# Kernel tuning notes

Hardware: AMD Instinct MI355X
Metric: run time of the kernel (lower is better)

Reference implementation:

```python
import jax, jax.numpy as jnp
import numpy as np

N = 32768       # total nodes = NUM_GRAPHS * T
F_IN = 32       # num_features
HC = 64         # hidden_channels
HEADS = 4
E = 524288      # edges before self-loops
NUM_GRAPHS = 64 # == batch.max()+1 by construction
T = 512         # time steps per graph (N // NUM_GRAPHS)
OUT = 24        # output_size
NEG_SLOPE = 0.2 # PyG GATConv default


def gat_layer(x, src, dst, W, a_src, a_dst, b, n_nodes):
    """PyG GATConv (concat=True) with edge softmax over incoming edges."""
    H, C = a_src.shape
    h = (x @ W).reshape(n_nodes, H, C)                    # [N,H,C]
    alpha_src = jnp.sum(h * a_src, axis=-1)               # [N,H]
    alpha_dst = jnp.sum(h * a_dst, axis=-1)               # [N,H]
    e = jax.nn.leaky_relu(alpha_src[src] + alpha_dst[dst], NEG_SLOPE)  # [E,H]
    m = jax.ops.segment_max(e, dst, num_segments=n_nodes)
    e = jnp.exp(e - m[dst])
    s = jax.ops.segment_sum(e, dst, num_segments=n_nodes)
    alpha = e / (s[dst] + 1e-16)                          # [E,H]
    msg = h[src] * alpha[..., None]                       # [E,H,C]
    out = jax.ops.segment_sum(msg, dst, num_segments=n_nodes)  # [N,H,C]
    return out.reshape(n_nodes, H * C) + b


def gru_layer(x, Wih, Whh, bih, bhh):
    """torch nn.GRU single layer, batch_first input x: [B,T,Hin] -> ([B,T,H], h_T)."""
    Bsz = x.shape[0]
    H = Whh.shape[1]

    def step(h, xt):
        gi = xt @ Wih.T + bih
        gh = h @ Whh.T + bhh
        ir, iz, inn = jnp.split(gi, 3, axis=-1)
        hr, hz, hn = jnp.split(gh, 3, axis=-1)
        r = jax.nn.sigmoid(ir + hr)
        z = jax.nn.sigmoid(iz + hz)
        n = jnp.tanh(inn + r * hn)
        h_new = (1.0 - z) * n + z * h
        return h_new, h_new

    h0 = jnp.zeros((Bsz, H), x.dtype)
    hT, ys = jax.lax.scan(step, h0, jnp.swapaxes(x, 0, 1))
    return jnp.swapaxes(ys, 0, 1), hT


def setup_inputs() -> dict:
    key = jax.random.key(0)
    ks = jax.random.split(key, 24)
    sc = 0.1
    inp = {
        "x": jax.random.normal(ks[0], (N, F_IN), dtype=jnp.float32),
        "edge_index": jax.random.randint(ks[1], (2, E), 0, N, dtype=jnp.int32),
        "batch": jnp.repeat(jnp.arange(NUM_GRAPHS, dtype=jnp.int32), T),
        # GAT layer 1: F_IN -> HC x HEADS (concat)
        "W1": sc * jax.random.normal(ks[2], (F_IN, HEADS * HC), dtype=jnp.float32),
        "a_src1": sc * jax.random.normal(ks[3], (HEADS, HC), dtype=jnp.float32),
        "a_dst1": sc * jax.random.normal(ks[4], (HEADS, HC), dtype=jnp.float32),
        "b1": jnp.zeros((HEADS * HC,), dtype=jnp.float32),
        # GAT layer 2: HEADS*HC -> HC, 1 head
        "W2": sc * jax.random.normal(ks[5], (HEADS * HC, HC), dtype=jnp.float32),
        "a_src2": sc * jax.random.normal(ks[6], (1, HC), dtype=jnp.float32),
        "a_dst2": sc * jax.random.normal(ks[7], (1, HC), dtype=jnp.float32),
        "b2": jnp.zeros((HC,), dtype=jnp.float32),
        # GRU (2 layers, input_size == hidden_size == HC)
        "gru_Wih0": sc * jax.random.normal(ks[8], (3 * HC, HC), dtype=jnp.float32),
        "gru_Whh0": sc * jax.random.normal(ks[9], (3 * HC, HC), dtype=jnp.float32),
        "gru_bih0": jnp.zeros((3 * HC,), dtype=jnp.float32),
        "gru_bhh0": jnp.zeros((3 * HC,), dtype=jnp.float32),
        "gru_Wih1": sc * jax.random.normal(ks[10], (3 * HC, HC), dtype=jnp.float32),
        "gru_Whh1": sc * jax.random.normal(ks[11], (3 * HC, HC), dtype=jnp.float32),
        "gru_bih1": jnp.zeros((3 * HC,), dtype=jnp.float32),
        "gru_bhh1": jnp.zeros((3 * HC,), dtype=jnp.float32),
        # Linear head
        "Wl": sc * jax.random.normal(ks[12], (OUT, HC), dtype=jnp.float32),
        "bl": jnp.zeros((OUT,), dtype=jnp.float32),
    }
    return inp


def reference(x, edge_index, batch, W1, a_src1, a_dst1, b1, W2, a_src2, a_dst2, b2,
              gru_Wih0, gru_Whh0, gru_bih0, gru_bhh0,
              gru_Wih1, gru_Whh1, gru_bih1, gru_bhh1, Wl, bl):
    # PyG GATConv default add_self_loops=True
    loops = jnp.arange(N, dtype=edge_index.dtype)
    src = jnp.concatenate([edge_index[0], loops])
    dst = jnp.concatenate([edge_index[1], loops])

    h = jax.nn.elu(gat_layer(x, src, dst, W1, a_src1, a_dst1, b1, N))   # [N, HEADS*HC]
    h = jax.nn.elu(gat_layer(h, src, dst, W2, a_src2, a_dst2, b2, N))   # [N, HC]

    # batch is repeat(arange(NUM_GRAPHS), T) so batch.max()+1 == NUM_GRAPHS (static)
    seq = h.reshape(NUM_GRAPHS, T, HC)
    seq, _ = gru_layer(seq, gru_Wih0, gru_Whh0, gru_bih0, gru_bhh0)
    _, hT = gru_layer(seq, gru_Wih1, gru_Whh1, gru_bih1, gru_bhh1)      # [B, HC]
    return hT @ Wl.T + bl                                               # [B, OUT]
```

## Files before the change

kernel.cpp:

```cpp
#include <hip/hip_runtime.h>
#include <hip/hip_bf16.h>

#define N_NODES 32768
#define F_IN    32
#define HC      64
#define HEADS   4
#define NE      524288
#define NET     (NE + N_NODES)
#define NG      64
#define TT      512
#define OUTF    24

__device__ __forceinline__ float lrelu(float x){ return x > 0.f ? x : 0.2f*x; }
__device__ __forceinline__ float eluf (float x){ return x > 0.f ? x : __expf(x)-1.f; }
__device__ __forceinline__ float sigmf(float x){ return 1.f/(1.f+__expf(-x)); }
__device__ __forceinline__ float tanhfast(float x){ return 1.f - 2.f/(__expf(2.f*x)+1.f); }
__device__ __forceinline__ float bcast(float v, int k){
  return __int_as_float(__builtin_amdgcn_readlane(__float_as_int(v), k));
}

__global__ __launch_bounds__(256) void k_deg(const int* __restrict__ ei,
                                             int* __restrict__ deg){
  int e = blockIdx.x*256 + threadIdx.x;
  int d = (e < NE) ? ei[NE+e] : (e - NE);
  atomicAdd(deg + d, 1);
}

__global__ __launch_bounds__(1024) void k_scan(const int* __restrict__ deg,
                                               int* __restrict__ rowptr){
  __shared__ int ps[1024];
  const int t = threadIdx.x;
  const int base = t*32;
  int local[32]; int s = 0;
  #pragma unroll
  for(int i=0;i<32;i++){ local[i]=deg[base+i]; s+=local[i]; }
  ps[t]=s; __syncthreads();
  for(int off=1; off<1024; off<<=1){
    int v = (t>=off) ? ps[t-off] : 0;
    __syncthreads();
    ps[t]+=v;
    __syncthreads();
  }
  int run = (t==0) ? 0 : ps[t-1];
  #pragma unroll
  for(int i=0;i<32;i++){ rowptr[base+i]=run; run+=local[i]; }
  if(t==1023) rowptr[N_NODES]=run;
}

__global__ __launch_bounds__(256) void k_fill(const int* __restrict__ ei,
                                              const int* __restrict__ rowptr,
                                              int* __restrict__ cur,
                                              int* __restrict__ col){
  int e = blockIdx.x*256 + threadIdx.x;
  int s, d;
  if(e < NE){ s = ei[e]; d = ei[NE+e]; } else { s = e-NE; d = s; }
  int pos = atomicAdd(cur + d, 1);
  col[rowptr[d] + pos] = s;
}

__global__ __launch_bounds__(256) void k_prep(const float* __restrict__ W1,
                                              const float* __restrict__ a_src,
                                              const float* __restrict__ a_dst,
                                              float* __restrict__ p){
  const int t = threadIdx.x;
  const int k = t>>3, q = t&7;
  const int h = q>>1, isd = q&1;
  const float* av = (isd ? a_dst : a_src) + h*64;
  const float* wr = W1 + k*256 + h*64;
  float acc = 0.f;
  #pragma unroll
  for(int c=0;c<64;c++) acc += wr[c]*av[c];
  p[(isd?128:0) + k*4 + h] = acc;
}

__global__ __launch_bounds__(256) void k_alpha1x(const float* __restrict__ x,
                                                 const float* __restrict__ p,
                                                 float* __restrict__ as1,
                                                 float* __restrict__ ad1){
  __shared__ float ps[256];
  const int tid = threadIdx.x;
  ps[tid] = p[tid];
  __syncthreads();
  const int n = blockIdx.x*256 + tid;
  const float4* xr = (const float4*)(x + n*32);
  float sa0=0.f,sa1=0.f,sa2=0.f,sa3=0.f, sd0=0.f,sd1=0.f,sd2=0.f,sd3=0.f;
  #pragma unroll
  for(int k4=0;k4<8;k4++){
    float4 v = xr[k4];
    const float* pa = ps + (4*k4)*4;
    const float* pd = ps + 128 + (4*k4)*4;
    sa0 += v.x*pa[0] + v.y*pa[4] + v.z*pa[8]  + v.w*pa[12];
    sa1 += v.x*pa[1] + v.y*pa[5] + v.z*pa[9]  + v.w*pa[13];
    sa2 += v.x*pa[2] + v.y*pa[6] + v.z*pa[10] + v.w*pa[14];
    sa3 += v.x*pa[3] + v.y*pa[7] + v.z*pa[11] + v.w*pa[15];
    sd0 += v.x*pd[0] + v.y*pd[4] + v.z*pd[8]  + v.w*pd[12];
    sd1 += v.x*pd[1] + v.y*pd[5] + v.z*pd[9]  + v.w*pd[13];
    sd2 += v.x*pd[2] + v.y*pd[6] + v.z*pd[10] + v.w*pd[14];
    sd3 += v.x*pd[3] + v.y*pd[7] + v.z*pd[11] + v.w*pd[15];
  }
  *(float4*)(as1+n*4) = make_float4(sa0,sa1,sa2,sa3);
  *(float4*)(ad1+n*4) = make_float4(sd0,sd1,sd2,sd3);
}

__global__ __launch_bounds__(256) void k_gatx(const int* __restrict__ rowptr,
                                              const int* __restrict__ col,
                                              const float* __restrict__ as1,
                                              const float* __restrict__ ad1,
                                              const float* __restrict__ x,
                                              float* __restrict__ agg,
                                              float* __restrict__ s14){
  const int node = blockIdx.x*4 + (threadIdx.x>>6);
  const int lane = threadIdx.x & 63;
  const int h0   = lane>>5;
  const int c    = lane & 31;
  const int beg = rowptr[node], end = rowptr[node+1];
  const float adA = ad1[node*4 + h0];
  const float adB = ad1[node*4 + h0 + 2];
  float accA=0.f, accB=0.f, wsA=0.f, wsB=0.f;
  int j = beg;
  for(; j+1 < end; j += 2){
    int s0 = col[j], s1 = col[j+1];
    float4 q0 = *(const float4*)(as1 + s0*4);
    float4 q1 = *(const float4*)(as1 + s1*4);
    float aA0 = h0 ? q0.y : q0.x, aB0 = h0 ? q0.w : q0.z;
    float aA1 = h0 ? q1.y : q1.x, aB1 = h0 ? q1.w : q1.z;
    float wA0 = __expf(lrelu(aA0 + adA));
    float wB0 = __expf(lrelu(aB0 + adB));
    float wA1 = __expf(lrelu(aA1 + adA));
    float wB1 = __expf(lrelu(aB1 + adB));
    float x0 = x[s0*32 + c];
    float x1 = x[s1*32 + c];
    accA += wA0*x0 + wA1*x1;
    accB += wB0*x0 + wB1*x1;
    wsA  += wA0 + wA1;
    wsB  += wB0 + wB1;
  }
  if(j < end){
    int s0 = col[j];
    float4 q0 = *(const float4*)(as1 + s0*4);
    float aA0 = h0 ? q0.y : q0.x, aB0 = h0 ? q0.w : q0.z;
    float wA0 = __expf(lrelu(aA0 + adA));
    float wB0 = __expf(lrelu(aB0 + adB));
    float x0 = x[s0*32 + c];
    accA += wA0*x0; accB += wB0*x0;
    wsA += wA0; wsB += wB0;
  }
  agg[node*128 + h0*32 + c]     = accA;
  agg[node*128 + (h0+2)*32 + c] = accB;
  if(c == 0){
    s14[node*4 + h0]     = wsA;
    s14[node*4 + h0 + 2] = wsB;
  }
}

__global__ __launch_bounds__(256) void k_gemm1e(const float* __restrict__ agg,
                                                const float* __restrict__ W1,
                                                const float* __restrict__ s14,
                                                const float* __restrict__ b1,
                                                float* __restrict__ out1){
  __shared__ __align__(16) float ags[64*128];
  __shared__ __align__(16) float wsh[32*256];
  __shared__ float sv[64*4];
  const int tid = threadIdx.x;
  const int row0 = blockIdx.x*64;
  const float4* ag = (const float4*)(agg + row0*128);
  float4* ags4 = (float4*)ags;
  for(int i=tid;i<2048;i+=256) ags4[i]=ag[i];
  const float4* wg=(const float4*)W1; float4* ws4=(float4*)wsh;
  for(int i=tid;i<2048;i+=256) ws4[i]=wg[i];
  const float4* sg=(const float4*)(s14 + row0*4);
  float4* sv4=(float4*)sv;
  if(tid<64) sv4[tid]=sg[tid];
  __syncthreads();
  const int h = tid>>6;
  float wc[32];
  #pragma unroll
  for(int k=0;k<32;k++) wc[k]=wsh[k*256 + tid];
  const float bb = b1[tid];
  for(int r=0;r<64;r++){
    const float4* ar=(const float4*)(ags + r*128 + h*32);
    float acc=0.f;
    #pragma unroll
    for(int k4=0;k4<8;k4++){
      float4 v=ar[k4];
      acc += v.x*wc[4*k4]+v.y*wc[4*k4+1]+v.z*wc[4*k4+2]+v.w*wc[4*k4+3];
    }
    float inv = 1.f/(sv[r*4+h] + 1e-16f);
    out1[(row0+r)*256 + tid] = eluf(acc*inv + bb);
  }
}

__global__ __launch_bounds__(256) void k_gemm2(const float* __restrict__ in,
                                               const float* __restrict__ W2,
                                               float* __restrict__ h2){
  __shared__ __align__(16) float xs[64*256];
  const int tid=threadIdx.x;
  const int row0=blockIdx.x*64;
  const float4* xg=(const float4*)(in + row0*256);
  float4* xs4=(float4*)xs;
  for(int i=tid;i<4096;i+=256) xs4[i]=xg[i];
  __syncthreads();
  const int c0=(tid&15)*4;
  const int r0=(tid>>4)*4;
  float acc[4][4]={};
  for(int k=0;k<256;k+=4){
    float wv[4][4];
    #pragma unroll
    for(int i=0;i<4;i++){
      float4 w=*(const float4*)(W2+(k+i)*64+c0);
      wv[i][0]=w.x; wv[i][1]=w.y; wv[i][2]=w.z; wv[i][3]=w.w;
    }
    #pragma unroll
    for(int i=0;i<4;i++){
      float4 xv=*(const float4*)(xs+(r0+i)*256+k);
      #pragma unroll
      for(int j=0;j<4;j++)
        acc[i][j]+=xv.x*wv[0][j]+xv.y*wv[1][j]+xv.z*wv[2][j]+xv.w*wv[3][j];
    }
  }
  #pragma unroll
  for(int i=0;i<4;i++)
    *(float4*)(h2+(row0+r0+i)*64+c0)=make_float4(acc[i][0],acc[i][1],acc[i][2],acc[i][3]);
}

__global__ __launch_bounds__(256) void k_alpha2(const float* __restrict__ h2,
                                                const float* __restrict__ a_src,
                                                const float* __restrict__ a_dst,
                                                float* __restrict__ as2,
                                                float* __restrict__ ad2){
  int n = blockIdx.x*256 + threadIdx.x;
  const float4* hp=(const float4*)(h2+n*64);
  float sa=0.f, sd=0.f;
  #pragma unroll
  for(int i=0;i<16;i++){
    float4 v=hp[i];
    float4 a=((const float4*)a_src)[i];
    float4 d=((const float4*)a_dst)[i];
    sa+=v.x*a.x+v.y*a.y+v.z*a.z+v.w*a.w;
    sd+=v.x*d.x+v.y*d.y+v.z*d.z+v.w*d.w;
  }
  as2[n]=sa; ad2[n]=sd;
}

__global__ __launch_bounds__(256) void k_gat2(const int* __restrict__ rowptr,
                                              const int* __restrict__ col,
                                              const float* __restrict__ as2,
                                              const float* __restrict__ ad2,
                                              const float* __restrict__ h2,
                                              const float* __restrict__ b2,
                                              float* __restrict__ out2){
  const int node = blockIdx.x*4 + (threadIdx.x>>6);
  const int lane = threadIdx.x & 63;
  const int beg = rowptr[node], end = rowptr[node+1];
  const float ad = ad2[node];
  float acc = 0.f, s = 0.f;
  int j = beg;
  for(; j+1 < end; j += 2){
    int s0 = col[j], s1 = col[j+1];
    float w0 = __expf(lrelu(as2[s0] + ad));
    float w1 = __expf(lrelu(as2[s1] + ad));
    acc += w0*h2[s0*64+lane] + w1*h2[s1*64+lane];
    s += w0 + w1;
  }
  if(j < end){
    int s0 = col[j];
    float w0 = __expf(lrelu(as2[s0] + ad));
    acc += w0*h2[s0*64+lane];
    s += w0;
  }
  const float inv = 1.f/(s + 1e-16f);
  out2[node*64+lane] = eluf(acc*inv + b2[lane]);
}

__global__ __launch_bounds__(256) void k_gemm_gi(const float* __restrict__ in,
                                                 const float* __restrict__ Wih,
                                                 const float* __restrict__ bih,
                                                 float* __restrict__ gi){
  __shared__ __align__(16) float xs[64*64];
  __shared__ float wT[64*192];
  const int tid=threadIdx.x;
  const int row0=blockIdx.x*64;
  const float4* xg=(const float4*)(in+row0*64);
  float4* xs4=(float4*)xs;
  for(int i=tid;i<1024;i+=256) xs4[i]=xg[i];
  for(int i=tid;i<12288;i+=256){ wT[(i&63)*192+(i>>6)] = Wih[i]; }
  __syncthreads();
  if(tid<192){
    float wr[64];
    #pragma unroll
    for(int k=0;k<64;k++) wr[k]=wT[k*192+tid];
    const float bj=bih[tid];
    for(int r=0;r<64;r++){
      float acc=bj;
      const float4* xr=(const float4*)(xs+r*64);
      #pragma unroll
      for(int k4=0;k4<16;k4++){
        float4 v=xr[k4];
        acc+=v.x*wr[4*k4]+v.y*wr[4*k4+1]+v.z*wr[4*k4+2]+v.w*wr[4*k4+3];
      }
      gi[(row0+r)*192+tid]=acc;
    }
  }
}

__global__ __launch_bounds__(576,3) void k_gruR(const float* __restrict__ gi1,
                                                const float* __restrict__ Whh0,
                                                const float* __restrict__ bhh0,
                                                const float* __restrict__ Wih1,
                                                const float* __restrict__ bih1,
                                                const float* __restrict__ Whh1,
                                                const float* __restrict__ bhh1,
                                                const float* __restrict__ Wl,
                                                const float* __restrict__ bl,
                                                float* __restrict__ fout){
  __shared__ float h1s[64];
  __shared__ float h2s[64];
  __shared__ float gh1s[192];
  __shared__ float gi2s[192];
  __shared__ float gh2s[192];
  __shared__ float g1r[2][192];
  const int tid  = threadIdx.x;
  const int w    = tid >> 6;
  const int lane = tid & 63;
  const int b    = blockIdx.x;
  const float* gib = gi1 + (size_t)b*TT*192;

  const int crew = w/3;
  const int row  = (w%3)*64 + lane;
  const float* W  = (crew==0) ? Whh0 : (crew==1) ? Wih1 : Whh1;
  const float* bb = (crew==0) ? bhh0 : (crew==1) ? bih1 : bhh1;
  float* dst      = (crew==0) ? gh1s : (crew==1) ? gi2s : gh2s;

  const float4* wp = (const float4*)(W + row*64);
  float4 Wv0=wp[0],  Wv1=wp[1],  Wv2=wp[2],  Wv3=wp[3];
  float4 Wv4=wp[4],  Wv5=wp[5],  Wv6=wp[6],  Wv7=wp[7];
  float4 Wv8=wp[8],  Wv9=wp[9],  WvA=wp[10], WvB=wp[11];
  float4 WvC=wp[12], WvD=wp[13], WvE=wp[14], WvF=wp[15];
  const float bias = bb[row];

  float giv = 0.f;
  if(w < 3){
    g1r[0][row] = gib[row];
    giv = gib[192 + row];
  }
  if(tid < 64){ h1s[tid]=0.f; h2s[tid]=0.f; }
  __syncthreads();

  for(int i=0;i<=TT;i++){
    float hv = (crew==2) ? h2s[lane] : h1s[lane];
    if(w < 3){
      int pst = i+1;
      if(pst < TT) g1r[pst&1][row] = giv;
      int nst = i+2;
      if(nst < TT) giv = gib[nst*192 + row];
    }
    float a0=bias, a1=0.f, a2=0.f, a3=0.f;
#define DOT4(WV, BASE) \
    a0 = fmaf(bcast(hv, BASE+0), WV.x, a0); \
    a1 = fmaf(bcast(hv, BASE+1), WV.y, a1); \
    a2 = fmaf(bcast(hv, BASE+2), WV.z, a2); \
    a3 = fmaf(bcast(hv, BASE+3), WV.w, a3);
    DOT4(Wv0, 0)  DOT4(Wv1, 4)  DOT4(Wv2, 8)  DOT4(Wv3, 12)
    DOT4(Wv4, 16) DOT4(Wv5, 20) DOT4(Wv6, 24) DOT4(Wv7, 28)
    DOT4(Wv8, 32) DOT4(Wv9, 36) DOT4(WvA, 40) DOT4(WvB, 44)
    DOT4(WvC, 48) DOT4(WvD, 52) DOT4(WvE, 56) DOT4(WvF, 60)
#undef DOT4
    dst[row] = (a0+a1)+(a2+a3);
    __syncthreads();
    if(w == 0){
      if(i < TT){
        float r = sigmf(g1r[i&1][lane]     + gh1s[lane]);
        float z = sigmf(g1r[i&1][64+lane]  + gh1s[64+lane]);
        float n = tanhfast(g1r[i&1][128+lane] + r*gh1s[128+lane]);
        h1s[lane] = (1.f-z)*n + z*h1s[lane];
      }
    } else if(w == 3){
      if(i >= 1){
        float r = sigmf(gi2s[lane]     + gh2s[lane]);
        float z = sigmf(gi2s[64+lane]  + gh2s[64+lane]);
        float n = tanhfast(gi2s[128+lane] + r*gh2s[128+lane]);
        h2s[lane] = (1.f-z)*n + z*h2s[lane];
      }
    }
    __syncthreads();
  }

  if(tid < 24){
    float acc = bl[tid];
    const float4* wl4 = (const float4*)(Wl + tid*64);
    #pragma unroll
    for(int k4=0;k4<16;k4++){
      float4 h4 = *(const float4*)(h2s + 4*k4);
      float4 w4 = wl4[k4];
      acc += h4.x*w4.x + h4.y*w4.y + h4.z*w4.z + h4.w*w4.w;
    }
    fout[b*24+tid] = acc;
  }
}

extern "C" void kernel_launch(void* const* d_in, const int* in_sizes, int n_in,
                              void* d_out, int out_size, void* d_ws, size_t ws_size,
                              hipStream_t stream){
  const float* x     =(const float*)d_in[0];
  const int*   ei    =(const int*  )d_in[1];
  const float* W1    =(const float*)d_in[3];
  const float* a_src1=(const float*)d_in[4];
  const float* a_dst1=(const float*)d_in[5];
  const float* b1    =(const float*)d_in[6];
  const float* W2    =(const float*)d_in[7];
  const float* a_src2=(const float*)d_in[8];
  const float* a_dst2=(const float*)d_in[9];
  const float* b2    =(const float*)d_in[10];
  const float* Wih0  =(const float*)d_in[11];
  const float* Whh0  =(const float*)d_in[12];
  const float* bih0  =(const float*)d_in[13];
  const float* bhh0  =(const float*)d_in[14];
  const float* Wih1  =(const float*)d_in[15];
  const float* Whh1  =(const float*)d_in[16];
  const float* bih1  =(const float*)d_in[17];
  const float* bhh1  =(const float*)d_in[18];
  const float* Wl    =(const float*)d_in[19];
  const float* bl    =(const float*)d_in[20];

  float* ws   = (float*)d_ws;
  float* agg  = ws;
  float* s14  = ws + 4194304;
  float* gi   = ws;
  float* out1 = ws + 8388608;
  float* out2 = out1;
  float* h2   = ws + 16777216;
  float* as1  = ws + 18874368;
  float* ad1  = as1 + 131072;
  float* as2  = ad1 + 131072;
  float* ad2  = as2 + 32768;
  float* pbuf = ad2 + 32768;
  int* rowptr = (int*)(pbuf + 512);
  int* deg    = rowptr + 32800;
  int* cur    = deg + 32768;
  int* col    = cur + 32768;
  float* fo   = (float*)d_out;

  hipMemsetAsync(deg, 0, 2*32768*sizeof(int), stream);

  k_deg   <<<2176,256,0,stream>>>(ei,deg);
  k_scan  <<<1  ,1024,0,stream>>>(deg,rowptr);
  k_fill  <<<2176,256,0,stream>>>(ei,rowptr,cur,col);

  k_prep   <<<1   ,256,0,stream>>>(W1,a_src1,a_dst1,pbuf);
  k_alpha1x<<<128 ,256,0,stream>>>(x,pbuf,as1,ad1);
  k_gatx   <<<8192,256,0,stream>>>(rowptr,col,as1,ad1,x,agg,s14);
  k_gemm1e <<<512 ,256,0,stream>>>(agg,W1,s14,b1,out1);
  k_gemm2  <<<512 ,256,0,stream>>>(out1,W2,h2);
  k_alpha2 <<<128 ,256,0,stream>>>(h2,a_src2,a_dst2,as2,ad2);
  k_gat2   <<<8192,256,0,stream>>>(rowptr,col,as2,ad2,h2,b2,out2);
  k_gemm_gi<<<512 ,256,0,stream>>>(out2,Wih0,bih0,gi);
  k_gruR   <<<64  ,576,0,stream>>>(gi,Whh0,bhh0,Wih1,bih1,Whh1,bhh1,Wl,bl,fo);
  (void)in_sizes; (void)n_in; (void)out_size; (void)ws_size;
}
```

Before: 779.9 us.

## Fuse GAT layer-1 GEMM, layer-2 GEMM and alpha2; fold prep into alpha1; unroll gathers

Merges the layer-1 projection/ELU, the layer-2 GEMM and the layer-2 attention-coefficient computation into one kernel that keeps the 256-wide intermediate in shared memory, so it is never written to or read back from global memory. The weight/attention precompute is folded into the alpha1 kernel, and the edge-gather loops in both GAT aggregation kernels are unrolled by four to keep more loads in flight. Three kernel launches are removed. The cost is heavier shared-memory use per block, smaller row tiles and more register pressure in the gather loops.

```diff
diff --git a/kernel.cpp b/kernel.cpp
--- a/kernel.cpp
+++ b/kernel.cpp
@@ -58,28 +58,24 @@
   col[rowptr[d] + pos] = s;
 }
 
-__global__ __launch_bounds__(256) void k_prep(const float* __restrict__ W1,
-                                              const float* __restrict__ a_src,
-                                              const float* __restrict__ a_dst,
-                                              float* __restrict__ p){
-  const int t = threadIdx.x;
-  const int k = t>>3, q = t&7;
-  const int h = q>>1, isd = q&1;
-  const float* av = (isd ? a_dst : a_src) + h*64;
-  const float* wr = W1 + k*256 + h*64;
-  float acc = 0.f;
-  #pragma unroll
-  for(int c=0;c<64;c++) acc += wr[c]*av[c];
-  p[(isd?128:0) + k*4 + h] = acc;
-}
-
 __global__ __launch_bounds__(256) void k_alpha1x(const float* __restrict__ x,
-                                                 const float* __restrict__ p,
+                                                 const float* __restrict__ W1,
+                                                 const float* __restrict__ a_src,
+                                                 const float* __restrict__ a_dst,
                                                  float* __restrict__ as1,
                                                  float* __restrict__ ad1){
   __shared__ float ps[256];
   const int tid = threadIdx.x;
-  ps[tid] = p[tid];
+  {
+    const int k = tid>>3, q = tid&7;
+    const int h = q>>1, isd = q&1;
+    const float* av = (isd ? a_dst : a_src) + h*64;
+    const float* wr = W1 + k*256 + h*64;
+    float acc = 0.f;
+    #pragma unroll
+    for(int c=0;c<64;c++) acc += wr[c]*av[c];
+    ps[(isd?128:0) + k*4 + h] = acc;
+  }
   __syncthreads();
   const int n = blockIdx.x*256 + tid;
   const float4* xr = (const float4*)(x + n*32);
@@ -118,29 +114,34 @@
   const float adB = ad1[node*4 + h0 + 2];
   float accA=0.f, accB=0.f, wsA=0.f, wsB=0.f;
   int j = beg;
-  for(; j+1 < end; j += 2){
-    int s0 = col[j], s1 = col[j+1];
+  for(; j+3 < end; j += 4){
+    int s0 = col[j], s1 = col[j+1], s2 = col[j+2], s3 = col[j+3];
     float4 q0 = *(const float4*)(as1 + s0*4);
     float4 q1 = *(const float4*)(as1 + s1*4);
-    float aA0 = h0 ? q0.y : q0.x, aB0 = h0 ? q0.w : q0.z;
-    float aA1 = h0 ? q1.y : q1.x, aB1 = h0 ? q1.w : q1.z;
-    float wA0 = __expf(lrelu(aA0 + adA));
-    float wB0 = __expf(lrelu(aB0 + adB));
-    float wA1 = __expf(lrelu(aA1 + adA));
-    float wB1 = __expf(lrelu(aB1 + adB));
+    float4 q2 = *(const float4*)(as1 + s2*4);
+    float4 q3 = *(const float4*)(as1 + s3*4);
     float x0 = x[s0*32 + c];
     float x1 = x[s1*32 + c];
-    accA += wA0*x0 + wA1*x1;
-    accB += wB0*x0 + wB1*x1;
-    wsA  += wA0 + wA1;
-    wsB  += wB0 + wB1;
-  }
-  if(j < end){
+    float x2 = x[s2*32 + c];
+    float x3 = x[s3*32 + c];
+    float wA0 = __expf(lrelu((h0?q0.y:q0.x) + adA));
+    float wA1 = __expf(lrelu((h0?q1.y:q1.x) + adA));
+    float wA2 = __expf(lrelu((h0?q2.y:q2.x) + adA));
+    float wA3 = __expf(lrelu((h0?q3.y:q3.x) + adA));
+    float wB0 = __expf(lrelu((h0?q0.w:q0.z) + adB));
+    float wB1 = __expf(lrelu((h0?q1.w:q1.z) + adB));
+    float wB2 = __expf(lrelu((h0?q2.w:q2.z) + adB));
+    float wB3 = __expf(lrelu((h0?q3.w:q3.z) + adB));
+    accA += wA0*x0 + wA1*x1 + wA2*x2 + wA3*x3;
+    accB += wB0*x0 + wB1*x1 + wB2*x2 + wB3*x3;
+    wsA  += (wA0+wA1) + (wA2+wA3);
+    wsB  += (wB0+wB1) + (wB2+wB3);
+  }
+  for(; j < end; j++){
     int s0 = col[j];
     float4 q0 = *(const float4*)(as1 + s0*4);
-    float aA0 = h0 ? q0.y : q0.x, aB0 = h0 ? q0.w : q0.z;
-    float wA0 = __expf(lrelu(aA0 + adA));
-    float wB0 = __expf(lrelu(aB0 + adB));
+    float wA0 = __expf(lrelu((h0?q0.y:q0.x) + adA));
+    float wB0 = __expf(lrelu((h0?q0.w:q0.z) + adB));
     float x0 = x[s0*32 + c];
     accA += wA0*x0; accB += wB0*x0;
     wsA += wA0; wsB += wB0;
@@ -153,31 +154,32 @@
   }
 }
 
-__global__ __launch_bounds__(256) void k_gemm1e(const float* __restrict__ agg,
-                                                const float* __restrict__ W1,
-                                                const float* __restrict__ s14,
-                                                const float* __restrict__ b1,
-                                                float* __restrict__ out1){
-  __shared__ __align__(16) float ags[64*128];
-  __shared__ __align__(16) float wsh[32*256];
-  __shared__ float sv[64*4];
-  const int tid = threadIdx.x;
-  const int row0 = blockIdx.x*64;
-  const float4* ag = (const float4*)(agg + row0*128);
-  float4* ags4 = (float4*)ags;
-  for(int i=tid;i<2048;i+=256) ags4[i]=ag[i];
-  const float4* wg=(const float4*)W1; float4* ws4=(float4*)wsh;
-  for(int i=tid;i<2048;i+=256) ws4[i]=wg[i];
-  const float4* sg=(const float4*)(s14 + row0*4);
-  float4* sv4=(float4*)sv;
-  if(tid<64) sv4[tid]=sg[tid];
-  __syncthreads();
-  const int h = tid>>6;
+__global__ __launch_bounds__(256) void k_g12(const float* __restrict__ agg,
+                                             const float* __restrict__ W1,
+                                             const float* __restrict__ s14,
+                                             const float* __restrict__ b1,
+                                             const float* __restrict__ W2,
+                                             const float* __restrict__ a_src2,
+                                             const float* __restrict__ a_dst2,
+                                             float* __restrict__ h2,
+                                             float* __restrict__ as2,
+                                             float* __restrict__ ad2){
+  __shared__ __align__(16) float ags[32*128];
+  __shared__ __align__(16) float o1s[32*256];
+  __shared__ float sv[128];
+  const int tid  = threadIdx.x;
+  const int row0 = blockIdx.x*32;
+  const float4* ag = (const float4*)(agg + (size_t)row0*128);
+  float4* a4 = (float4*)ags;
+  for(int i=tid;i<1024;i+=256) a4[i]=ag[i];
+  if(tid<32) ((float4*)sv)[tid]=((const float4*)(s14+row0*4))[tid];
   float wc[32];
   #pragma unroll
-  for(int k=0;k<32;k++) wc[k]=wsh[k*256 + tid];
-  const float bb = b1[tid];
-  for(int r=0;r<64;r++){
+  for(int k=0;k<32;k++) wc[k]=W1[k*256+tid];
+  const float bb=b1[tid];
+  __syncthreads();
+  const int h = tid>>6;
+  for(int r=0;r<32;r++){
     const float4* ar=(const float4*)(ags + r*128 + h*32);
     float acc=0.f;
     #pragma unroll
@@ -186,23 +188,12 @@
       acc += v.x*wc[4*k4]+v.y*wc[4*k4+1]+v.z*wc[4*k4+2]+v.w*wc[4*k4+3];
     }
     float inv = 1.f/(sv[r*4+h] + 1e-16f);
-    out1[(row0+r)*256 + tid] = eluf(acc*inv + bb);
-  }
-}
-
-__global__ __launch_bounds__(256) void k_gemm2(const float* __restrict__ in,
-                                               const float* __restrict__ W2,
-                                               float* __restrict__ h2){
-  __shared__ __align__(16) float xs[64*256];
-  const int tid=threadIdx.x;
-  const int row0=blockIdx.x*64;
-  const float4* xg=(const float4*)(in + row0*256);
-  float4* xs4=(float4*)xs;
-  for(int i=tid;i<4096;i+=256) xs4[i]=xg[i];
+    o1s[r*256+tid] = eluf(acc*inv + bb);
+  }
   __syncthreads();
   const int c0=(tid&15)*4;
-  const int r0=(tid>>4)*4;
-  float acc[4][4]={};
+  const int r0=(tid>>4)*2;
+  float acc2[2][4]={};
   for(int k=0;k<256;k+=4){
     float wv[4][4];
     #pragma unroll
@@ -211,35 +202,34 @@
       wv[i][0]=w.x; wv[i][1]=w.y; wv[i][2]=w.z; wv[i][3]=w.w;
     }
     #pragma unroll
-    for(int i=0;i<4;i++){
-      float4 xv=*(const float4*)(xs+(r0+i)*256+k);
+    for(int i=0;i<2;i++){
+      float4 xv=*(const float4*)(o1s+(r0+i)*256+k);
       #pragma unroll
       for(int j=0;j<4;j++)
-        acc[i][j]+=xv.x*wv[0][j]+xv.y*wv[1][j]+xv.z*wv[2][j]+xv.w*wv[3][j];
-    }
-  }
+        acc2[i][j]+=xv.x*wv[0][j]+xv.y*wv[1][j]+xv.z*wv[2][j]+xv.w*wv[3][j];
+    }
+  }
+  float* h2s = ags;
   #pragma unroll
-  for(int i=0;i<4;i++)
-    *(float4*)(h2+(row0+r0+i)*64+c0)=make_float4(acc[i][0],acc[i][1],acc[i][2],acc[i][3]);
-}
-
-__global__ __launch_bounds__(256) void k_alpha2(const float* __restrict__ h2,
-                                                const float* __restrict__ a_src,
-                                                const float* __restrict__ a_dst,
-                                                float* __restrict__ as2,
-                                                float* __restrict__ ad2){
-  int n = blockIdx.x*256 + threadIdx.x;
-  const float4* hp=(const float4*)(h2+n*64);
-  float sa=0.f, sd=0.f;
-  #pragma unroll
-  for(int i=0;i<16;i++){
-    float4 v=hp[i];
-    float4 a=((const float4*)a_src)[i];
-    float4 d=((const float4*)a_dst)[i];
-    sa+=v.x*a.x+v.y*a.y+v.z*a.z+v.w*a.w;
-    sd+=v.x*d.x+v.y*d.y+v.z*d.z+v.w*d.w;
-  }
-  as2[n]=sa; ad2[n]=sd;
+  for(int i=0;i<2;i++){
+    float4 o = make_float4(acc2[i][0],acc2[i][1],acc2[i][2],acc2[i][3]);
+    *(float4*)(h2 + (size_t)(row0+r0+i)*64 + c0) = o;
+    *(float4*)(h2s + (r0+i)*64 + c0) = o;
+  }
+  __syncthreads();
+  if(tid < 32){
+    const float4* hp=(const float4*)(h2s + tid*64);
+    float sa=0.f, sd=0.f;
+    #pragma unroll
+    for(int i=0;i<16;i++){
+      float4 v=hp[i];
+      float4 a=((const float4*)a_src2)[i];
+      float4 d=((const float4*)a_dst2)[i];
+      sa+=v.x*a.x+v.y*a.y+v.z*a.z+v.w*a.w;
+      sd+=v.x*d.x+v.y*d.y+v.z*d.z+v.w*d.w;
+    }
+    as2[row0+tid]=sa; ad2[row0+tid]=sd;
+  }
 }
 
 __global__ __launch_bounds__(256) void k_gat2(const int* __restrict__ rowptr,
@@ -255,14 +245,19 @@
   const float ad = ad2[node];
   float acc = 0.f, s = 0.f;
   int j = beg;
-  for(; j+1 < end; j += 2){
-    int s0 = col[j], s1 = col[j+1];
-    float w0 = __expf(lrelu(as2[s0] + ad));
-    float w1 = __expf(lrelu(as2[s1] + ad));
-    acc += w0*h2[s0*64+lane] + w1*h2[s1*64+lane];
-    s += w0 + w1;
-  }
-  if(j < end){
+  for(; j+3 < end; j += 4){
+    int s0 = col[j], s1 = col[j+1], s2 = col[j+2], s3 = col[j+3];
+    float a0 = as2[s0], a1 = as2[s1], a2 = as2[s2], a3 = as2[s3];
+    float v0 = h2[s0*64+lane], v1 = h2[s1*64+lane];
+    float v2 = h2[s2*64+lane], v3 = h2[s3*64+lane];
+    float w0 = __expf(lrelu(a0 + ad));
+    float w1 = __expf(lrelu(a1 + ad));
+    float w2 = __expf(lrelu(a2 + ad));
+    float w3 = __expf(lrelu(a3 + ad));
+    acc += w0*v0 + w1*v1 + w2*v2 + w3*v3;
+    s += (w0+w1) + (w2+w3);
+  }
+  for(; j < end; j++){
     int s0 = col[j];
     float w0 = __expf(lrelu(as2[s0] + ad));
     acc += w0*h2[s0*64+lane];
@@ -426,15 +421,13 @@
   float* agg  = ws;
   float* s14  = ws + 4194304;
   float* gi   = ws;
-  float* out1 = ws + 8388608;
-  float* out2 = out1;
+  float* out2 = ws + 8388608;
   float* h2   = ws + 16777216;
   float* as1  = ws + 18874368;
   float* ad1  = as1 + 131072;
   float* as2  = ad1 + 131072;
   float* ad2  = as2 + 32768;
-  float* pbuf = ad2 + 32768;
-  int* rowptr = (int*)(pbuf + 512);
+  int* rowptr = (int*)(ad2 + 32768);
   int* deg    = rowptr + 32800;
   int* cur    = deg + 32768;
   int* col    = cur + 32768;
@@ -446,12 +439,9 @@
   k_scan  <<<1  ,1024,0,stream>>>(deg,rowptr);
   k_fill  <<<2176,256,0,stream>>>(ei,rowptr,cur,col);
 
-  k_prep   <<<1   ,256,0,stream>>>(W1,a_src1,a_dst1,pbuf);
-  k_alpha1x<<<128 ,256,0,stream>>>(x,pbuf,as1,ad1);
+  k_alpha1x<<<128 ,256,0,stream>>>(x,W1,a_src1,a_dst1,as1,ad1);
   k_gatx   <<<8192,256,0,stream>>>(rowptr,col,as1,ad1,x,agg,s14);
-  k_gemm1e <<<512 ,256,0,stream>>>(agg,W1,s14,b1,out1);
-  k_gemm2  <<<512 ,256,0,stream>>>(out1,W2,h2);
-  k_alpha2 <<<128 ,256,0,stream>>>(h2,a_src2,a_dst2,as2,ad2);
+  k_g12    <<<1024,256,0,stream>>>(agg,W1,s14,b1,W2,a_src2,a_dst2,h2,as2,ad2);
   k_gat2   <<<8192,256,0,stream>>>(rowptr,col,as2,ad2,h2,b2,out2);
   k_gemm_gi<<<512 ,256,0,stream>>>(out2,Wih0,bih0,gi);
   k_gruR   <<<64  ,576,0,stream>>>(gi,Whh0,bhh0,Wih1,bih1,Whh1,bhh1,Wl,bl,fo);
```

Measured after the change: 755.1 us (median of 2 runs). 3.2% less time.
